# Kernel tuning notes

Hardware: AMD Instinct MI355X
Metric: run time of the kernel (lower is better)

Reference implementation:

```python
import jax, jax.numpy as jnp
import numpy as np

B, N, C, NH = 8, 16384, 256, 8
CH = C // NH          # head dim = 32
SCALE = CH ** -0.5
HH = WW = 128         # N = HH*WW
# CoaT crpe window dict {3:2, 5:3, 7:3}: 2 heads->3x3, 3 heads->5x5, 3 heads->7x7


def setup_inputs() -> dict:
    key = jax.random.key(0)
    ks = jax.random.split(key, 9)
    w = lambda k, shp: (jax.random.normal(k, shp, jnp.float32) * 0.02)
    return {
        "x": jax.random.normal(ks[0], (B, N, C), jnp.float32),
        "w_qkv": w(ks[1], (C, 3 * C)),              # qkv_bias=False
        "w_proj": w(ks[2], (C, C)),
        "b_proj": jnp.zeros((C,), jnp.float32),
        "w3": w(ks[3], (3, 3, 1, 2 * CH)),          # HWIO depthwise, 2 heads
        "b3": jnp.zeros((2 * CH,), jnp.float32),
        "w5": w(ks[4], (5, 5, 1, 3 * CH)),          # 3 heads
        "b5": jnp.zeros((3 * CH,), jnp.float32),
        "w7": w(ks[5], (7, 7, 1, 3 * CH)),          # 3 heads
        "b7": jnp.zeros((3 * CH,), jnp.float32),
        "H": HH,
        "W": WW,
    }


def _hydra(q, k, v):
    # q,k,v: [B, h, N, Ch]; normalize over feature dim, O(N) token reduction
    qn = q * jax.lax.rsqrt(jnp.sum(q * q, axis=-1, keepdims=True))
    kn = k * jax.lax.rsqrt(jnp.sum(k * k, axis=-1, keepdims=True))
    kv = jnp.sum(kn * v, axis=-2, keepdims=True)   # [B, h, 1, Ch]
    return qn * kv                                  # broadcast over tokens


def _dwconv(img, kern, bias):
    # img: [B, c, H, W]; kern: [kh, kw, 1, c] (HWIO depthwise)
    c = img.shape[1]
    out = jax.lax.conv_general_dilated(
        img, kern, window_strides=(1, 1), padding="SAME",
        feature_group_count=c,
        dimension_numbers=("NCHW", "HWIO", "NCHW"))
    return out + bias[None, :, None, None]


def _crpe(q, v, Hs, Ws, convs):
    # CoaT ConvRelPosEnc: depthwise conv on v per head group, gated by q
    b, h, n, ch = v.shape
    outs, idx = [], 0
    for heads, kern, bias in convs:
        vs = v[:, idx:idx + heads]                          # [B, hs, N, Ch]
        v_img = vs.transpose(0, 1, 3, 2).reshape(b, heads * ch, Hs, Ws)
        cv = _dwconv(v_img, kern, bias)
        cv = cv.reshape(b, heads, ch, n).transpose(0, 1, 3, 2)
        outs.append(q[:, idx:idx + heads] * cv)
        idx += heads
    return jnp.concatenate(outs, axis=1)                    # [B, h, N, Ch]


def reference(x, w_qkv, w_proj, b_proj, w3, b3, w5, b5, w7, b7, H, W):
    b, n, c = x.shape
    qkv = (x @ w_qkv).reshape(b, n, 3, NH, CH).transpose(2, 0, 3, 1, 4)
    q, k, v = qkv[0], qkv[1], qkv[2]                        # [B, h, N, Ch]
    factor_att = _hydra(q, k, v)
    crpe = _crpe(q, v, H, W, [(2, w3, b3), (3, w5, b5), (3, w7, b7)])
    out = SCALE * factor_att + crpe
    out = out.transpose(0, 2, 1, 3).reshape(b, n, c)        # [B, N, C]
    return out @ w_proj + b_proj
```

## Files before the change

kernel.cpp:

```cpp
#include <hip/hip_runtime.h>
#include <hip/hip_bf16.h>


typedef __hip_bfloat16 bf16;
typedef __bf16 bf16x8 __attribute__((ext_vector_type(8)));
typedef unsigned short u16x8 __attribute__((ext_vector_type(8)));
typedef float f32x4 __attribute__((ext_vector_type(4)));
typedef float f32x8 __attribute__((ext_vector_type(8)));

#define SCALE_ 0.17677669529663687f

__device__ __forceinline__ unsigned short f2b(float f) {
  __hip_bfloat16 h = __float2bfloat16(f);
  return __builtin_bit_cast(unsigned short, h);
}
__device__ __forceinline__ float blo(unsigned u) {
  return __builtin_bit_cast(float, u << 16);
}
__device__ __forceinline__ float bhi(unsigned u) {
  return __builtin_bit_cast(float, u & 0xffff0000u);
}
__device__ __forceinline__ f32x8 unpack8(uint4 u) {
  f32x8 r;
  r[0] = blo(u.x); r[1] = bhi(u.x); r[2] = blo(u.y); r[3] = bhi(u.y);
  r[4] = blo(u.z); r[5] = bhi(u.z); r[6] = blo(u.w); r[7] = bhi(u.w);
  return r;
}
__device__ __forceinline__ uint4 pack8v(const f32x8 o) {
  uint4 s;
  s.x = (unsigned)f2b(o[0]) | ((unsigned)f2b(o[1]) << 16);
  s.y = (unsigned)f2b(o[2]) | ((unsigned)f2b(o[3]) << 16);
  s.z = (unsigned)f2b(o[4]) | ((unsigned)f2b(o[5]) << 16);
  s.w = (unsigned)f2b(o[6]) | ((unsigned)f2b(o[7]) << 16);
  return s;
}
__device__ __forceinline__ void gload16(const void* g, void* l) {
  __builtin_amdgcn_global_load_lds(
      (const __attribute__((address_space(1))) unsigned int*)g,
      (__attribute__((address_space(3))) unsigned int*)l, 16, 0, 0);
}
__device__ __forceinline__ f32x4 mfma16(u16x8 a, u16x8 b, f32x4 c) {
  return __builtin_amdgcn_mfma_f32_16x16x32_bf16(
      __builtin_bit_cast(bf16x8, a), __builtin_bit_cast(bf16x8, b), c, 0, 0, 0);
}
__device__ __forceinline__ void barrier_vm4() {
  asm volatile("s_waitcnt vmcnt(4) lgkmcnt(0)" ::: "memory");
  __builtin_amdgcn_s_barrier();
  asm volatile("" ::: "memory");
}
__device__ __forceinline__ void barrier_vm0() {
  asm volatile("s_waitcnt vmcnt(0) lgkmcnt(0)" ::: "memory");
  __builtin_amdgcn_s_barrier();
  asm volatile("" ::: "memory");
}
__device__ __forceinline__ void fma8(f32x8& a, const f32x8 v, const float4 w0,
                                     const float4 w1) {
  a[0] += v[0] * w0.x; a[1] += v[1] * w0.y;
  a[2] += v[2] * w0.z; a[3] += v[3] * w0.w;
  a[4] += v[4] * w1.x; a[5] += v[5] * w1.y;
  a[6] += v[6] * w1.z; a[7] += v[7] * w1.w;
}

__global__ __launch_bounds__(256) void prep_weights(
    const float* __restrict__ wqkv, const float* __restrict__ wproj,
    bf16* __restrict__ wqkvT, bf16* __restrict__ wprojT) {
  const int idx = blockIdx.x * 256 + threadIdx.x;
  if (idx < 768 * 256) {
    const int j = idx >> 8, k = idx & 255;
    wqkvT[idx] = __float2bfloat16(wqkv[k * 768 + j]);
  }
  if (idx < 256 * 256) {
    const int j = idx >> 8, k = idx & 255;
    wprojT[idx] = __float2bfloat16(wproj[k * 256 + j]);
  }
}

__global__ __launch_bounds__(256) void prep_x(const float* __restrict__ x,
                                              bf16* __restrict__ xb) {
  const size_t idx = ((size_t)blockIdx.x * 256 + threadIdx.x) * 8;
  const float4 a0 = *(const float4*)(x + idx);
  const float4 a1 = *(const float4*)(x + idx + 4);
  u16x8 p;
  p[0] = f2b(a0.x); p[1] = f2b(a0.y); p[2] = f2b(a0.z); p[3] = f2b(a0.w);
  p[4] = f2b(a1.x); p[5] = f2b(a1.y); p[6] = f2b(a1.z); p[7] = f2b(a1.w);
  *(u16x8*)(xb + idx) = p;
}

__global__ __launch_bounds__(256) void qkv_mfma(
    const bf16* __restrict__ xb, const bf16* __restrict__ wT,
    bf16* __restrict__ qO, bf16* __restrict__ kO, bf16* __restrict__ vO) {
  __shared__ __align__(16) char LDSU[49152];
  char* As = LDSU;
  char* Bs = LDSU + 24576;
  const int tid = threadIdx.x;
  const int l = tid & 63, w = tid >> 6;
  const int wr = w >> 1, wc = w & 1;

  const int lin = blockIdx.y * 6 + blockIdx.x;
  const int xcd = lin & 7, qq = lin >> 3;
  const int jt = qq % 6;
  const int ttile = xcd * 128 + qq / 6;
  const int j0 = jt << 7;
  const int t0 = ttile << 7;
  const int b = t0 >> 14;
  const int n0 = t0 & 16383;

  f32x4 acc[4][4];
#pragma unroll
  for (int m = 0; m < 4; ++m)
#pragma unroll
    for (int t = 0; t < 4; ++t) acc[m][t] = (f32x4){0.f, 0.f, 0.f, 0.f};

  const int row0 = w * 16 + (l >> 2), row1 = row0 + 64;
  const int sl = l & 3;
  const int sw0 = (row0 >> 1) & 3, sw1 = (row1 >> 1) & 3;
  const bf16* asrc0 = wT + (size_t)(j0 + row0) * 256 + ((sl ^ sw0) << 3);
  const bf16* asrc1 = wT + (size_t)(j0 + row1) * 256 + ((sl ^ sw1) << 3);
  const bf16* bsrc0 = xb + (size_t)(t0 + row0) * 256 + ((sl ^ sw0) << 3);
  const bf16* bsrc1 = xb + (size_t)(t0 + row1) * 256 + ((sl ^ sw1) << 3);
  const int d0 = w * 1024, d1 = 4096 + w * 1024;

  const int fr = l & 15;
  const int fq = l >> 4;
  const int fs = (fq ^ ((l >> 1) & 3)) << 4;

  gload16(asrc0, As + d0);
  gload16(asrc1, As + d1);
  gload16(bsrc0, Bs + d0);
  gload16(bsrc1, Bs + d1);
  gload16(asrc0 + 32, As + 8192 + d0);
  gload16(asrc1 + 32, As + 8192 + d1);
  gload16(bsrc0 + 32, Bs + 8192 + d0);
  gload16(bsrc1 + 32, Bs + 8192 + d1);
  barrier_vm4();

#pragma unroll
  for (int t = 0; t < 8; ++t) {
    if (t < 6) {
      const int kn = (t + 2) << 5;
      const int nb = ((t + 2) % 3) * 8192;
      gload16(asrc0 + kn, As + nb + d0);
      gload16(asrc1 + kn, As + nb + d1);
      gload16(bsrc0 + kn, Bs + nb + d0);
      gload16(bsrc1 + kn, Bs + nb + d1);
    }
    const char* Ac = As + (t % 3) * 8192;
    const char* Bc = Bs + (t % 3) * 8192;
    u16x8 af[4], bfv[4];
#pragma unroll
    for (int m = 0; m < 4; ++m)
      af[m] = *(const u16x8*)(Ac + (wr * 64 + m * 16 + fr) * 64 + fs);
#pragma unroll
    for (int tt = 0; tt < 4; ++tt)
      bfv[tt] = *(const u16x8*)(Bc + (wc * 64 + tt * 16 + fr) * 64 + fs);
    __builtin_amdgcn_s_setprio(1);
#pragma unroll
    for (int m = 0; m < 4; ++m)
#pragma unroll
      for (int tt = 0; tt < 4; ++tt)
        acc[m][tt] = mfma16(af[m], bfv[tt], acc[m][tt]);
    __builtin_amdgcn_s_setprio(0);
    if (t < 6) barrier_vm4();
    else if (t < 7) barrier_vm0();
  }
  __syncthreads();

#pragma unroll
  for (int m = 0; m < 4; ++m) {
    const int jq = wr * 16 + m * 4 + fq;
#pragma unroll
    for (int t = 0; t < 4; ++t) {
      const int token = wc * 64 + t * 16 + fr;
      const int p = jq ^ (token & 15);
      uint2 pk;
      pk.x = (unsigned)f2b(acc[m][t][0]) | ((unsigned)f2b(acc[m][t][1]) << 16);
      pk.y = (unsigned)f2b(acc[m][t][2]) | ((unsigned)f2b(acc[m][t][3]) << 16);
      *(uint2*)(LDSU + token * 256 + (p << 3)) = pk;
    }
  }
  __syncthreads();

  const int region = j0 >> 8;
  bf16* outp = (region == 0) ? qO : ((region == 1) ? kO : vO);
  const int jl = j0 & 255;
  const int seg = tid & 15;
#pragma unroll
  for (int r = 0; r < 8; ++r) {
    const int token = r * 16 + (tid >> 4);
    const int tsw = token & 15;
    const uint2 lo = *(const uint2*)(LDSU + token * 256 + (((2 * seg) ^ tsw) << 3));
    const uint2 hi =
        *(const uint2*)(LDSU + token * 256 + (((2 * seg + 1) ^ tsw) << 3));
    uint4 d;
    d.x = lo.x; d.y = lo.y; d.z = hi.x; d.w = hi.y;
    *(uint4*)&outp[((size_t)b * 16384 + n0 + token) * 256 + jl + seg * 8] = d;
  }
}

__global__ __launch_bounds__(256) void kv_reduce(
    const bf16* __restrict__ kT, const bf16* __restrict__ vT,
    float* __restrict__ kv) {
  __shared__ float red[256 * 8];
  const int tid = threadIdx.x;
  const int b = blockIdx.y;
  const int seg = tid & 31;
  f32x8 part = (f32x8)0.f;

  for (int r = 0; r < 32; ++r) {
    const int token = blockIdx.x * 256 + r * 8 + (tid >> 5);
    const size_t roff = ((size_t)b * 16384 + token) * 256;
    const uint4 kd = *(const uint4*)(kT + roff + seg * 8);
    const f32x8 kf = unpack8(kd);
    float ss = 0.f;
#pragma unroll
    for (int i = 0; i < 8; ++i) ss += kf[i] * kf[i];
    ss += __shfl_xor(ss, 1);
    ss += __shfl_xor(ss, 2);
    const float inv = rsqrtf(ss);
    const uint4 vd = *(const uint4*)(vT + roff + seg * 8);
    const f32x8 vf = unpack8(vd);
#pragma unroll
    for (int i = 0; i < 8; ++i) part[i] += kf[i] * inv * vf[i];
  }
#pragma unroll
  for (int i = 0; i < 8; ++i) red[tid * 8 + i] = part[i];
  __syncthreads();
  if (tid < 32) {
    f32x8 s = (f32x8)0.f;
#pragma unroll
    for (int k = 0; k < 8; ++k)
#pragma unroll
      for (int i = 0; i < 8; ++i) s[i] += red[(tid + 32 * k) * 8 + i];
#pragma unroll
    for (int i = 0; i < 8; ++i)
      atomicAdd(&kv[b * 256 + seg * 8 + i], s[i]);
  }
}

template <int K>
__global__ __launch_bounds__(256) void crpe_conv(
    const bf16* __restrict__ qT, const bf16* __restrict__ vT,
    const float* __restrict__ kvbuf, const float* __restrict__ wp,
    const float* __restrict__ bp, int OC, int hbase,
    bf16* __restrict__ mid) {
  constexpr int R = K / 2;
  constexpr int SY = 16 + 2 * R;
  constexpr int SXr = 32 + 2 * R;
  constexpr int SX = SXr + 1;
  constexpr int PL = SX * SY;
  __shared__ __align__(16) uint4 vs[4 * PL];
  __shared__ float wlds[K * K * 32];
  __shared__ float blds[32];

  const int tid = threadIdx.x;
  const int hg = blockIdx.x;
  const int h = hbase + hg;
  const int tile = blockIdx.y;
  const int b = blockIdx.z;
  const int tx0 = (tile & 3) * 32, ty0 = (tile >> 2) * 16;
  const int tx = tid & 15, ty = tid >> 4;
  const int ocbase = hg * 32;

  {
    const int cc = tid & 3;
    for (int e = tid >> 2; e < SXr * SY; e += 64) {
      const int ly = e / SXr, lx = e - ly * SXr;
      const int gy = ty0 - R + ly, gx = tx0 - R + lx;
      uint4 d = {0, 0, 0, 0};
      if (gy >= 0 && gy < 128 && gx >= 0 && gx < 128)
        d = *((const uint4*)(vT + ((size_t)b * 16384 + gy * 128 + gx) * 256 +
                             h * 32) + cc);
      vs[cc * PL + ly * SX + lx] = d;
    }
  }
  for (int e = tid; e < K * K * 32; e += 256)
    wlds[e] = wp[(e >> 5) * OC + ocbase + (e & 31)];
  if (tid < 32) blds[tid] = bp[ocbase + tid];
  __syncthreads();

  const int n = (ty0 + ty) * 128 + tx0 + 2 * tx;
  const size_t off0 = ((size_t)b * 16384 + n) * 256 + h * 32;
  const uint4* q0 = (const uint4*)(qT + off0);
  const uint4* q1 = (const uint4*)(qT + off0 + 256);
  float ss0 = 0.f, ss1 = 0.f;
#pragma unroll
  for (int cc = 0; cc < 4; ++cc) {
    const f32x8 a = unpack8(q0[cc]);
    const f32x8 c = unpack8(q1[cc]);
#pragma unroll
    for (int i = 0; i < 8; ++i) { ss0 += a[i] * a[i]; ss1 += c[i] * c[i]; }
  }
  const float qinv0 = rsqrtf(ss0), qinv1 = rsqrtf(ss1);
  const float4* kvp = (const float4*)(kvbuf + ((size_t)b * 8 + h) * 32);
  const float4* wlds4 = (const float4*)wlds;
  const float4* bl4 = (const float4*)blds;
  uint4* m0 = (uint4*)(mid + off0);
  uint4* m1 = (uint4*)(mid + off0 + 256);

#pragma unroll 1
  for (int cc = 0; cc < 4; ++cc) {
    const uint4* vplane = vs + cc * PL;
    const float4 ba = bl4[cc * 2], bb = bl4[cc * 2 + 1];
    f32x8 a0, a1;
    a0[0] = ba.x; a0[1] = ba.y; a0[2] = ba.z; a0[3] = ba.w;
    a0[4] = bb.x; a0[5] = bb.y; a0[6] = bb.z; a0[7] = bb.w;
    a1 = a0;
#pragma unroll
    for (int ky = 0; ky < K; ++ky) {
      const uint4* vrow = vplane + (ty + ky) * SX + 2 * tx;
      f32x8 vcur = unpack8(vrow[0]);
#pragma unroll
      for (int kx = 0; kx < K; ++kx) {
        const f32x8 vnx = unpack8(vrow[kx + 1]);
        const float4 w0 = wlds4[(ky * K + kx) * 8 + cc * 2];
        const float4 w1 = wlds4[(ky * K + kx) * 8 + cc * 2 + 1];
        fma8(a0, vcur, w0, w1);
        fma8(a1, vnx, w0, w1);
        vcur = vnx;
      }
    }
    const float4 ka = kvp[cc * 2], kb = kvp[cc * 2 + 1];
    f32x8 kvf;
    kvf[0] = ka.x; kvf[1] = ka.y; kvf[2] = ka.z; kvf[3] = ka.w;
    kvf[4] = kb.x; kvf[5] = kb.y; kvf[6] = kb.z; kvf[7] = kb.w;
    {
      const f32x8 qv = unpack8(q0[cc]);
      f32x8 o;
#pragma unroll
      for (int i = 0; i < 8; ++i)
        o[i] = SCALE_ * qv[i] * qinv0 * kvf[i] + qv[i] * a0[i];
      m0[cc] = pack8v(o);
    }
    {
      const f32x8 qv = unpack8(q1[cc]);
      f32x8 o;
#pragma unroll
      for (int i = 0; i < 8; ++i)
        o[i] = SCALE_ * qv[i] * qinv1 * kvf[i] + qv[i] * a1[i];
      m1[cc] = pack8v(o);
    }
  }
}

__global__ __launch_bounds__(256) void proj_mfma(
    const bf16* __restrict__ mid, const bf16* __restrict__ wpT,
    const float* __restrict__ bproj, float* __restrict__ out) {
  __shared__ __align__(16) char LDSU[49152];
  char* As = LDSU;
  char* Bs = LDSU + 24576;
  const int tid = threadIdx.x;
  const int l = tid & 63, w = tid >> 6;
  const int wr = w >> 1, wc = w & 1;

  const int lin = blockIdx.y * 2 + blockIdx.x;
  const int xcd = lin & 7, qq = lin >> 3;
  const int jt = qq & 1;
  const int ttile = xcd * 128 + (qq >> 1);
  const int j0 = jt << 7;
  const int tk0 = ttile << 7;

  f32x4 acc[4][4];
#pragma unroll
  for (int m = 0; m < 4; ++m)
#pragma unroll
    for (int t = 0; t < 4; ++t) acc[m][t] = (f32x4){0.f, 0.f, 0.f, 0.f};

  const int row0 = w * 16 + (l >> 2), row1 = row0 + 64;
  const int sl = l & 3;
  const int sw0 = (row0 >> 1) & 3, sw1 = (row1 >> 1) & 3;
  const bf16* asrc0 = wpT + (size_t)(j0 + row0) * 256 + ((sl ^ sw0) << 3);
  const bf16* asrc1 = wpT + (size_t)(j0 + row1) * 256 + ((sl ^ sw1) << 3);
  const bf16* bsrc0 = mid + (size_t)(tk0 + row0) * 256 + ((sl ^ sw0) << 3);
  const bf16* bsrc1 = mid + (size_t)(tk0 + row1) * 256 + ((sl ^ sw1) << 3);
  const int d0 = w * 1024, d1 = 4096 + w * 1024;

  const int fr = l & 15;
  const int fq = l >> 4;
  const int fs = (fq ^ ((l >> 1) & 3)) << 4;

  gload16(asrc0, As + d0);
  gload16(asrc1, As + d1);
  gload16(bsrc0, Bs + d0);
  gload16(bsrc1, Bs + d1);
  gload16(asrc0 + 32, As + 8192 + d0);
  gload16(asrc1 + 32, As + 8192 + d1);
  gload16(bsrc0 + 32, Bs + 8192 + d0);
  gload16(bsrc1 + 32, Bs + 8192 + d1);
  barrier_vm4();

#pragma unroll
  for (int t = 0; t < 8; ++t) {
    if (t < 6) {
      const int kn = (t + 2) << 5;
      const int nb = ((t + 2) % 3) * 8192;
      gload16(asrc0 + kn, As + nb + d0);
      gload16(asrc1 + kn, As + nb + d1);
      gload16(bsrc0 + kn, Bs + nb + d0);
      gload16(bsrc1 + kn, Bs + nb + d1);
    }
    const char* Ac = As + (t % 3) * 8192;
    const char* Bc = Bs + (t % 3) * 8192;
    u16x8 af[4], bfv[4];
#pragma unroll
    for (int m = 0; m < 4; ++m)
      af[m] = *(const u16x8*)(Ac + (wr * 64 + m * 16 + fr) * 64 + fs);
#pragma unroll
    for (int tt = 0; tt < 4; ++tt)
      bfv[tt] = *(const u16x8*)(Bc + (wc * 64 + tt * 16 + fr) * 64 + fs);
    __builtin_amdgcn_s_setprio(1);
#pragma unroll
    for (int m = 0; m < 4; ++m)
#pragma unroll
      for (int tt = 0; tt < 4; ++tt)
        acc[m][tt] = mfma16(af[m], bfv[tt], acc[m][tt]);
    __builtin_amdgcn_s_setprio(0);
    if (t < 6) barrier_vm4();
    else if (t < 7) barrier_vm0();
  }
  __syncthreads();

#pragma unroll
  for (int m = 0; m < 4; ++m) {
    const float4 bias = *(const float4*)&bproj[j0 + wr * 64 + m * 16 + fq * 4];
#pragma unroll
    for (int t = 0; t < 4; ++t) {
      acc[m][t][0] += bias.x;
      acc[m][t][1] += bias.y;
      acc[m][t][2] += bias.z;
      acc[m][t][3] += bias.w;
    }
  }

  for (int chunk = 0; chunk < 2; ++chunk) {
    if (wc == chunk) {
#pragma unroll
      for (int m = 0; m < 4; ++m) {
        const int jq = wr * 16 + m * 4 + fq;
#pragma unroll
        for (int t = 0; t < 4; ++t) {
          const int ltok = t * 16 + fr;
          const int p = jq ^ (ltok & 15);
          float4 r;
          r.x = acc[m][t][0]; r.y = acc[m][t][1];
          r.z = acc[m][t][2]; r.w = acc[m][t][3];
          *(float4*)(LDSU + ltok * 512 + (p << 4)) = r;
        }
      }
    }
    __syncthreads();
    const int seg = tid & 31;
#pragma unroll
    for (int r = 0; r < 8; ++r) {
      const int ltok = r * 8 + (tid >> 5);
      const int p = seg ^ (ltok & 15);
      const float4 dv = *(const float4*)(LDSU + ltok * 512 + (p << 4));
      *(float4*)&out[(size_t)(tk0 + chunk * 64 + ltok) * 256 + j0 + seg * 4] = dv;
    }
    __syncthreads();
  }
}

extern "C" void kernel_launch(void* const* d_in, const int* in_sizes, int n_in,
                              void* d_out, int out_size, void* d_ws,
                              size_t ws_size, hipStream_t stream) {
  const float* x     = (const float*)d_in[0];
  const float* wqkv  = (const float*)d_in[1];
  const float* wproj = (const float*)d_in[2];
  const float* bproj = (const float*)d_in[3];
  const float* w3 = (const float*)d_in[4];
  const float* b3 = (const float*)d_in[5];
  const float* w5 = (const float*)d_in[6];
  const float* b5 = (const float*)d_in[7];
  const float* w7 = (const float*)d_in[8];
  const float* b7 = (const float*)d_in[9];
  float* out = (float*)d_out;

  const size_t PLANE = (size_t)8 * 16384 * 256;
  bf16* qT  = (bf16*)d_ws;
  bf16* vT  = qT + PLANE;
  bf16* kT  = vT + PLANE;
  bf16* mid = kT;
  float* kv = (float*)(kT + PLANE);
  bf16* wqkvT  = (bf16*)(kv + 2048);
  bf16* wprojT = wqkvT + 768 * 256;
  bf16* xb = (bf16*)d_out;

  hipMemsetAsync(kv, 0, 2048 * sizeof(float), stream);
  prep_weights<<<dim3(768), 256, 0, stream>>>(wqkv, wproj, wqkvT, wprojT);
  prep_x<<<dim3(16384), 256, 0, stream>>>(x, xb);
  qkv_mfma<<<dim3(6, 1024), 256, 0, stream>>>(xb, wqkvT, qT, kT, vT);
  kv_reduce<<<dim3(64, 8), 256, 0, stream>>>(kT, vT, kv);
  crpe_conv<3><<<dim3(2, 32, 8), 256, 0, stream>>>(qT, vT, kv, w3, b3, 64, 0, mid);
  crpe_conv<5><<<dim3(3, 32, 8), 256, 0, stream>>>(qT, vT, kv, w5, b5, 96, 2, mid);
  crpe_conv<7><<<dim3(3, 32, 8), 256, 0, stream>>>(qT, vT, kv, w7, b7, 96, 5, mid);
  proj_mfma<<<dim3(2, 1024), 256, 0, stream>>>(mid, wprojT, bproj, out);
}
```

Baseline: 353.9 us.

## Merge prep and crpe launches, halve conv LDS tile, widen kv_reduce grid

Folds the x and weight conversion kernels into one launch. The three per-window-size depthwise conv kernels become a single launch that dispatches on head index. The conv stages its v tile in two halves of two channel-chunks each, which halves LDS use per block so more blocks can be resident, at the cost of extra barriers and a second staging pass. kv_reduce now uses four times as many blocks, each covering fewer tokens, to raise parallelism, which in turn multiplies the number of atomics.

Result: slower. 435.5 us (+23.1%).

```diff
diff --git a/kernel.cpp b/kernel.cpp
--- a/kernel.cpp
+++ b/kernel.cpp
@@ -61,29 +61,30 @@
   a[6] += v[6] * w1.z; a[7] += v[7] * w1.w;
 }
 
-__global__ __launch_bounds__(256) void prep_weights(
-    const float* __restrict__ wqkv, const float* __restrict__ wproj,
+__global__ __launch_bounds__(256) void prep_all(
+    const float* __restrict__ x, const float* __restrict__ wqkv,
+    const float* __restrict__ wproj, bf16* __restrict__ xb,
     bf16* __restrict__ wqkvT, bf16* __restrict__ wprojT) {
-  const int idx = blockIdx.x * 256 + threadIdx.x;
-  if (idx < 768 * 256) {
-    const int j = idx >> 8, k = idx & 255;
-    wqkvT[idx] = __float2bfloat16(wqkv[k * 768 + j]);
-  }
-  if (idx < 256 * 256) {
-    const int j = idx >> 8, k = idx & 255;
-    wprojT[idx] = __float2bfloat16(wproj[k * 256 + j]);
-  }
-}
-
-__global__ __launch_bounds__(256) void prep_x(const float* __restrict__ x,
-                                              bf16* __restrict__ xb) {
-  const size_t idx = ((size_t)blockIdx.x * 256 + threadIdx.x) * 8;
-  const float4 a0 = *(const float4*)(x + idx);
-  const float4 a1 = *(const float4*)(x + idx + 4);
-  u16x8 p;
-  p[0] = f2b(a0.x); p[1] = f2b(a0.y); p[2] = f2b(a0.z); p[3] = f2b(a0.w);
-  p[4] = f2b(a1.x); p[5] = f2b(a1.y); p[6] = f2b(a1.z); p[7] = f2b(a1.w);
-  *(u16x8*)(xb + idx) = p;
+  const int bid = blockIdx.x;
+  if (bid < 16384) {
+    const size_t idx = ((size_t)bid * 256 + threadIdx.x) * 8;
+    const float4 a0 = *(const float4*)(x + idx);
+    const float4 a1 = *(const float4*)(x + idx + 4);
+    u16x8 p;
+    p[0] = f2b(a0.x); p[1] = f2b(a0.y); p[2] = f2b(a0.z); p[3] = f2b(a0.w);
+    p[4] = f2b(a1.x); p[5] = f2b(a1.y); p[6] = f2b(a1.z); p[7] = f2b(a1.w);
+    *(u16x8*)(xb + idx) = p;
+  } else {
+    const int idx = (bid - 16384) * 256 + threadIdx.x;
+    if (idx < 768 * 256) {
+      const int j = idx >> 8, k = idx & 255;
+      wqkvT[idx] = __float2bfloat16(wqkv[k * 768 + j]);
+    }
+    if (idx < 256 * 256) {
+      const int j = idx >> 8, k = idx & 255;
+      wprojT[idx] = __float2bfloat16(wproj[k * 256 + j]);
+    }
+  }
 }
 
 __global__ __launch_bounds__(256) void qkv_mfma(
@@ -206,8 +207,8 @@
   const int seg = tid & 31;
   f32x8 part = (f32x8)0.f;
 
-  for (int r = 0; r < 32; ++r) {
-    const int token = blockIdx.x * 256 + r * 8 + (tid >> 5);
+  for (int r = 0; r < 8; ++r) {
+    const int token = blockIdx.x * 64 + r * 8 + (tid >> 5);
     const size_t roff = ((size_t)b * 16384 + token) * 256;
     const uint4 kd = *(const uint4*)(kT + roff + seg * 8);
     const f32x8 kf = unpack8(kd);
@@ -238,45 +239,27 @@
 }
 
 template <int K>
-__global__ __launch_bounds__(256) void crpe_conv(
+__device__ __forceinline__ void crpe_impl(
+    uint4* __restrict__ vs, float* __restrict__ wlds, float* __restrict__ blds,
     const bf16* __restrict__ qT, const bf16* __restrict__ vT,
     const float* __restrict__ kvbuf, const float* __restrict__ wp,
-    const float* __restrict__ bp, int OC, int hbase,
+    const float* __restrict__ bp, int OC, int hg, int h,
     bf16* __restrict__ mid) {
   constexpr int R = K / 2;
   constexpr int SY = 16 + 2 * R;
   constexpr int SXr = 32 + 2 * R;
   constexpr int SX = SXr + 1;
   constexpr int PL = SX * SY;
-  __shared__ __align__(16) uint4 vs[4 * PL];
-  __shared__ float wlds[K * K * 32];
-  __shared__ float blds[32];
-
   const int tid = threadIdx.x;
-  const int hg = blockIdx.x;
-  const int h = hbase + hg;
   const int tile = blockIdx.y;
   const int b = blockIdx.z;
   const int tx0 = (tile & 3) * 32, ty0 = (tile >> 2) * 16;
   const int tx = tid & 15, ty = tid >> 4;
   const int ocbase = hg * 32;
 
-  {
-    const int cc = tid & 3;
-    for (int e = tid >> 2; e < SXr * SY; e += 64) {
-      const int ly = e / SXr, lx = e - ly * SXr;
-      const int gy = ty0 - R + ly, gx = tx0 - R + lx;
-      uint4 d = {0, 0, 0, 0};
-      if (gy >= 0 && gy < 128 && gx >= 0 && gx < 128)
-        d = *((const uint4*)(vT + ((size_t)b * 16384 + gy * 128 + gx) * 256 +
-                             h * 32) + cc);
-      vs[cc * PL + ly * SX + lx] = d;
-    }
-  }
   for (int e = tid; e < K * K * 32; e += 256)
     wlds[e] = wp[(e >> 5) * OC + ocbase + (e & 31)];
   if (tid < 32) blds[tid] = bp[ocbase + tid];
-  __syncthreads();
 
   const int n = (ty0 + ty) * 128 + tx0 + 2 * tx;
   const size_t off0 = ((size_t)b * 16384 + n) * 256 + h * 32;
@@ -298,48 +281,86 @@
   uint4* m1 = (uint4*)(mid + off0 + 256);
 
 #pragma unroll 1
-  for (int cc = 0; cc < 4; ++cc) {
-    const uint4* vplane = vs + cc * PL;
-    const float4 ba = bl4[cc * 2], bb = bl4[cc * 2 + 1];
-    f32x8 a0, a1;
-    a0[0] = ba.x; a0[1] = ba.y; a0[2] = ba.z; a0[3] = ba.w;
-    a0[4] = bb.x; a0[5] = bb.y; a0[6] = bb.z; a0[7] = bb.w;
-    a1 = a0;
-#pragma unroll
-    for (int ky = 0; ky < K; ++ky) {
-      const uint4* vrow = vplane + (ty + ky) * SX + 2 * tx;
-      f32x8 vcur = unpack8(vrow[0]);
-#pragma unroll
-      for (int kx = 0; kx < K; ++kx) {
-        const f32x8 vnx = unpack8(vrow[kx + 1]);
-        const float4 w0 = wlds4[(ky * K + kx) * 8 + cc * 2];
-        const float4 w1 = wlds4[(ky * K + kx) * 8 + cc * 2 + 1];
-        fma8(a0, vcur, w0, w1);
-        fma8(a1, vnx, w0, w1);
-        vcur = vnx;
+  for (int half = 0; half < 2; ++half) {
+    __syncthreads();
+    {
+      const int ccl = tid & 1;
+      const int cc = 2 * half + ccl;
+      for (int e = tid >> 1; e < SXr * SY; e += 128) {
+        const int ly = e / SXr, lx = e - ly * SXr;
+        const int gy = ty0 - R + ly, gx = tx0 - R + lx;
+        uint4 d = {0, 0, 0, 0};
+        if (gy >= 0 && gy < 128 && gx >= 0 && gx < 128)
+          d = *((const uint4*)(vT + ((size_t)b * 16384 + gy * 128 + gx) * 256 +
+                               h * 32) + cc);
+        vs[ccl * PL + ly * SX + lx] = d;
       }
     }
-    const float4 ka = kvp[cc * 2], kb = kvp[cc * 2 + 1];
-    f32x8 kvf;
-    kvf[0] = ka.x; kvf[1] = ka.y; kvf[2] = ka.z; kvf[3] = ka.w;
-    kvf[4] = kb.x; kvf[5] = kb.y; kvf[6] = kb.z; kvf[7] = kb.w;
-    {
-      const f32x8 qv = unpack8(q0[cc]);
-      f32x8 o;
-#pragma unroll
-      for (int i = 0; i < 8; ++i)
-        o[i] = SCALE_ * qv[i] * qinv0 * kvf[i] + qv[i] * a0[i];
-      m0[cc] = pack8v(o);
-    }
-    {
-      const f32x8 qv = unpack8(q1[cc]);
-      f32x8 o;
-#pragma unroll
-      for (int i = 0; i < 8; ++i)
-        o[i] = SCALE_ * qv[i] * qinv1 * kvf[i] + qv[i] * a1[i];
-      m1[cc] = pack8v(o);
-    }
-  }
+    __syncthreads();
+#pragma unroll
+    for (int ccl = 0; ccl < 2; ++ccl) {
+      const int cc = 2 * half + ccl;
+      const uint4* vplane = vs + ccl * PL;
+      const float4 ba = bl4[cc * 2], bb = bl4[cc * 2 + 1];
+      f32x8 a0, a1;
+      a0[0] = ba.x; a0[1] = ba.y; a0[2] = ba.z; a0[3] = ba.w;
+      a0[4] = bb.x; a0[5] = bb.y; a0[6] = bb.z; a0[7] = bb.w;
+      a1 = a0;
+#pragma unroll
+      for (int ky = 0; ky < K; ++ky) {
+        const uint4* vrow = vplane + (ty + ky) * SX + 2 * tx;
+        f32x8 vcur = unpack8(vrow[0]);
+#pragma unroll
+        for (int kx = 0; kx < K; ++kx) {
+          const f32x8 vnx = unpack8(vrow[kx + 1]);
+          const float4 w0 = wlds4[(ky * K + kx) * 8 + cc * 2];
+          const float4 w1 = wlds4[(ky * K + kx) * 8 + cc * 2 + 1];
+          fma8(a0, vcur, w0, w1);
+          fma8(a1, vnx, w0, w1);
+          vcur = vnx;
+        }
+      }
+      const float4 ka = kvp[cc * 2], kb = kvp[cc * 2 + 1];
+      f32x8 kvf;
+      kvf[0] = ka.x; kvf[1] = ka.y; kvf[2] = ka.z; kvf[3] = ka.w;
+      kvf[4] = kb.x; kvf[5] = kb.y; kvf[6] = kb.z; kvf[7] = kb.w;
+      {
+        const f32x8 qv = unpack8(q0[cc]);
+        f32x8 o;
+#pragma unroll
+        for (int i = 0; i < 8; ++i)
+          o[i] = SCALE_ * qv[i] * qinv0 * kvf[i] + qv[i] * a0[i];
+        m0[cc] = pack8v(o);
+      }
+      {
+        const f32x8 qv = unpack8(q1[cc]);
+        f32x8 o;
+#pragma unroll
+        for (int i = 0; i < 8; ++i)
+          o[i] = SCALE_ * qv[i] * qinv1 * kvf[i] + qv[i] * a1[i];
+        m1[cc] = pack8v(o);
+      }
+    }
+  }
+}
+
+__global__ __launch_bounds__(256) void crpe_all(
+    const bf16* __restrict__ qT, const bf16* __restrict__ vT,
+    const float* __restrict__ kvbuf,
+    const float* __restrict__ w3, const float* __restrict__ b3,
+    const float* __restrict__ w5, const float* __restrict__ b5,
+    const float* __restrict__ w7, const float* __restrict__ b7,
+    bf16* __restrict__ mid) {
+  __shared__ __align__(16) uint4 vs[2 * 39 * 22];
+  __shared__ float wlds[49 * 32];
+  __shared__ float blds[32];
+  const int h = blockIdx.x;
+  if (h < 2)
+    crpe_impl<3>(vs, wlds, blds, qT, vT, kvbuf, w3, b3, 64, h, h, mid);
+  else if (h < 5)
+    crpe_impl<5>(vs, wlds, blds, qT, vT, kvbuf, w5, b5, 96, h - 2, h, mid);
+  else
+    crpe_impl<7>(vs, wlds, blds, qT, vT, kvbuf, w7, b7, 96, h - 5, h, mid);
 }
 
 __global__ __launch_bounds__(256) void proj_mfma(
@@ -486,12 +507,11 @@
   bf16* xb = (bf16*)d_out;
 
   hipMemsetAsync(kv, 0, 2048 * sizeof(float), stream);
-  prep_weights<<<dim3(768), 256, 0, stream>>>(wqkv, wproj, wqkvT, wprojT);
-  prep_x<<<dim3(16384), 256, 0, stream>>>(x, xb);
+  prep_all<<<dim3(16384 + 768), 256, 0, stream>>>(x, wqkv, wproj, xb, wqkvT,
+                                                  wprojT);
   qkv_mfma<<<dim3(6, 1024), 256, 0, stream>>>(xb, wqkvT, qT, kT, vT);
-  kv_reduce<<<dim3(64, 8), 256, 0, stream>>>(kT, vT, kv);
-  crpe_conv<3><<<dim3(2, 32, 8), 256, 0, stream>>>(qT, vT, kv, w3, b3, 64, 0, mid);
-  crpe_conv<5><<<dim3(3, 32, 8), 256, 0, stream>>>(qT, vT, kv, w5, b5, 96, 2, mid);
-  crpe_conv<7><<<dim3(3, 32, 8), 256, 0, stream>>>(qT, vT, kv, w7, b7, 96, 5, mid);
+  kv_reduce<<<dim3(256, 8), 256, 0, stream>>>(kT, vT, kv);
+  crpe_all<<<dim3(8, 32, 8), 256, 0, stream>>>(qT, vT, kv, w3, b3, w5, b5, w7,
+                                               b7, mid);
   proj_mfma<<<dim3(2, 1024), 256, 0, stream>>>(mid, wprojT, bproj, out);
 }
```
